# Kernel optimization log

Measured on AMD Instinct MI355X. Metric: run time of the kernel, lower is better.

## Reference

```python
import jax, jax.numpy as jnp
import numpy as np

N_POI = 100000   # number of POIs
N_EDGE = 50000   # directed hyperedges
N_USER = 50000   # user hyperedges (multi-view)
NNZ = 1_000_000  # nonzeros per incidence matrix
D = 128          # embedding dim
L = 3            # num_layers


def spmm(rows, cols, vals, x, num_rows):
    """COO sparse @ dense: y[r] += vals * x[c]."""
    return jax.ops.segment_sum(vals[:, None] * x[cols], rows, num_segments=num_rows)


def hyper_net(pois, rows1, cols1, vals1, n1, rows2, cols2, vals2, n2, attn):
    """Chained two-hop sparse propagation with relu + residual, layer-attention fusion.
    Dropout omitted (eval mode / deterministic reference)."""
    embs = [pois]
    x = pois
    for _ in range(L):
        m = spmm(rows1, cols1, vals1, x, n1)      # [n1, D] aggregate to hyperedges/users
        m = spmm(rows2, cols2, vals2, m, n2)      # [N_POI, D] propagate back to POIs
        x = jax.nn.relu(m) + embs[-1]             # relu + residual
        embs.append(x)
    w = jax.nn.softmax(attn)                      # [L+1]
    return jnp.einsum('l,lnd->nd', w, jnp.stack(embs))


def setup_inputs() -> dict:
    key = jax.random.key(0)
    ks = jax.random.split(key, 16)
    inp = {
        'pois_embs': jax.random.normal(ks[0], (N_POI, D), dtype=jnp.float32),
        'tar_rows': jax.random.randint(ks[1], (NNZ,), 0, N_EDGE, dtype=jnp.int32),
        'tar_cols': jax.random.randint(ks[2], (NNZ,), 0, N_POI, dtype=jnp.int32),
        'tar_vals': jax.random.uniform(ks[3], (NNZ,), dtype=jnp.float32),
        'src_rows': jax.random.randint(ks[4], (NNZ,), 0, N_POI, dtype=jnp.int32),
        'src_cols': jax.random.randint(ks[5], (NNZ,), 0, N_EDGE, dtype=jnp.int32),
        'src_vals': jax.random.uniform(ks[6], (NNZ,), dtype=jnp.float32),
        'up_rows': jax.random.randint(ks[7], (NNZ,), 0, N_USER, dtype=jnp.int32),
        'up_cols': jax.random.randint(ks[8], (NNZ,), 0, N_POI, dtype=jnp.int32),
        'up_vals': jax.random.uniform(ks[9], (NNZ,), dtype=jnp.float32),
        'pu_rows': jax.random.randint(ks[10], (NNZ,), 0, N_POI, dtype=jnp.int32),
        'pu_cols': jax.random.randint(ks[11], (NNZ,), 0, N_USER, dtype=jnp.int32),
        'pu_vals': jax.random.uniform(ks[12], (NNZ,), dtype=jnp.float32),
        'attn_di': jnp.ones((L + 1,), dtype=jnp.float32),
        'attn_mv': jnp.ones((L + 1,), dtype=jnp.float32),
    }
    return inp


def reference(pois_embs, tar_rows, tar_cols, tar_vals, src_rows, src_cols, src_vals,
              up_rows, up_cols, up_vals, pu_rows, pu_cols, pu_vals, attn_di, attn_mv):
    # Directed hypergraph branch: msg_tar = HG_poi_tar @ x ; msg_src = HG_poi_src @ msg_tar
    di = hyper_net(pois_embs, tar_rows, tar_cols, tar_vals, N_EDGE,
                   src_rows, src_cols, src_vals, N_POI, attn_di)
    # Multi-view (user) hypergraph branch: HG_up @ x ; HG_pu @ msg
    mv = hyper_net(pois_embs, up_rows, up_cols, up_vals, N_USER,
                   pu_rows, pu_cols, pu_vals, N_POI, attn_mv)
    return di + mv
```

## Files before the change

### kernel.cpp

```cpp
#include <hip/hip_runtime.h>

#define NNZC   1000000
#define NPOI   100000
#define NEDGE  50000
#define NUSER  50000
#define DIM    128
#define NL     3

#define PB     128
#define NBKT   196
#define SCANN  (4 * NBKT * PB)

static inline int ceil_div(int a, int b) { return (a + b - 1) / b; }

typedef unsigned int uint32;

__device__ __forceinline__ float bfLO(uint32 u) { return __uint_as_float(u << 16); }
__device__ __forceinline__ float bfHI(uint32 u) { return __uint_as_float(u & 0xffff0000u); }
__device__ __forceinline__ uint32 bf16_rne(float f) {
    uint32 u = __float_as_uint(f);
    return (u + 0x7fffu + ((u >> 16) & 1u)) >> 16;
}
__device__ __forceinline__ uint32 bfPACK(float a, float b) {
    return bf16_rne(a) | (bf16_rne(b) << 16);
}
__device__ __forceinline__ uint32 csrPACK(int col, float val) {
    return ((uint32)col) | (bf16_rne(val) << 17);
}
__device__ __forceinline__ int   csrCOL(uint32 e) { return (int)(e & 0x1FFFFu); }
__device__ __forceinline__ float csrVAL(uint32 e) { return __uint_as_float((e >> 17) << 16); }

__device__ __constant__ const int c_nrows[4]  = { NEDGE, NPOI, NUSER, NPOI };
__device__ __constant__ const int c_cntoff[4] = { 0, NEDGE, NEDGE + NPOI, NEDGE + NPOI + NUSER };
__device__ __constant__ const int c_cap[4]    = { 64, 48, 64, 48 };
__device__ __constant__ const int c_shift[4]  = { 8, 9, 8, 9 };
__device__ __constant__ const long long c_elloff[4] = { 0, 3200000, 8000000, 11200000 };


__global__ __launch_bounds__(1024) void histH_kernel(
    const int* __restrict__ r0, const int* __restrict__ r1,
    const int* __restrict__ r2, const int* __restrict__ r3,
    int* __restrict__ histG) {
    __shared__ int h[NBKT];
    int m = blockIdx.y, p = blockIdx.x;
    for (int i = threadIdx.x; i < NBKT; i += 1024) h[i] = 0;
    __syncthreads();
    const int* r = (m == 0) ? r0 : (m == 1) ? r1 : (m == 2) ? r2 : r3;
    int shift = c_shift[m];
    int lo = (int)(((long long)NNZC * p) >> 7);
    int hi = (int)(((long long)NNZC * (p + 1)) >> 7);
    for (int i = lo + (int)threadIdx.x; i < hi; i += 1024)
        atomicAdd(&h[r[i] >> shift], 1);
    __syncthreads();
    for (int b = threadIdx.x; b < NBKT; b += 1024)
        histG[(m * NBKT + b) * PB + p] = h[b];
}

__global__ __launch_bounds__(256) void scan_kernel(int* __restrict__ g) {
    __shared__ int base[257];
    int t = threadIdx.x;
    const int chunk = SCANN / 256;
    int lo = t * chunk;
    int s = 0;
    for (int i = 0; i < chunk; i++) s += g[lo + i];
    base[t + 1] = s;
    __syncthreads();
    if (t == 0) {
        base[0] = 0;
        for (int i = 1; i <= 256; i++) base[i] += base[i - 1];
    }
    __syncthreads();
    int off = base[t];
    for (int i = 0; i < chunk; i++) { int v = g[lo + i]; g[lo + i] = off; off += v; }
    if (t == 255) g[SCANN] = base[256];
}

__global__ __launch_bounds__(1024) void scatS_kernel(
    const int* __restrict__ r0, const int* __restrict__ r1,
    const int* __restrict__ r2, const int* __restrict__ r3,
    const int* __restrict__ c0, const int* __restrict__ c1,
    const int* __restrict__ c2, const int* __restrict__ c3,
    const float* __restrict__ v0, const float* __restrict__ v1,
    const float* __restrict__ v2, const float* __restrict__ v3,
    const int* __restrict__ scanG, uint2* __restrict__ rec) {
    __shared__ int cur[NBKT];
    int m = blockIdx.y, p = blockIdx.x;
    for (int b = threadIdx.x; b < NBKT; b += 1024)
        cur[b] = scanG[(m * NBKT + b) * PB + p];
    __syncthreads();
    const int*   r = (m == 0) ? r0 : (m == 1) ? r1 : (m == 2) ? r2 : r3;
    const int*   c = (m == 0) ? c0 : (m == 1) ? c1 : (m == 2) ? c2 : c3;
    const float* v = (m == 0) ? v0 : (m == 1) ? v1 : (m == 2) ? v2 : v3;
    int shift = c_shift[m];
    int lo = (int)(((long long)NNZC * p) >> 7);
    int hi = (int)(((long long)NNZC * (p + 1)) >> 7);
    for (int i = lo + (int)threadIdx.x; i < hi; i += 1024) {
        int row = r[i];
        int pos = atomicAdd(&cur[row >> shift], 1);
        rec[pos] = make_uint2((uint32)row, csrPACK(c[i], v[i]));
    }
}

__global__ __launch_bounds__(512) void fillB_kernel(
    const int* __restrict__ scanG, const uint2* __restrict__ rec,
    int* __restrict__ counts_all, uint32* __restrict__ ell) {
    __shared__ int cnt[512];
    int bx = (int)blockIdx.x;
    int m = bx / NBKT, b = bx - m * NBKT;
    int shift = c_shift[m];
    int rowlo = b << shift;
    int bklen = 1 << shift;
    for (int i = threadIdx.x; i < bklen; i += 512) cnt[i] = 0;
    __syncthreads();
    int lo = scanG[(m * NBKT + b) * PB];
    int hi = scanG[(m * NBKT + b + 1) * PB];
    int cap = c_cap[m];
    uint32* ebase = ell + c_elloff[m];
    for (int i = lo + (int)threadIdx.x; i < hi; i += 512) {
        uint2 e = rec[i];
        int row = (int)e.x;
        int pos = atomicAdd(&cnt[row - rowlo], 1);
        ebase[(size_t)row * cap + pos] = e.y;
    }
    __syncthreads();
    int nrows_b = c_nrows[m] - rowlo;
    if (nrows_b > bklen) nrows_b = bklen;
    int* counts = counts_all + c_cntoff[m];
    for (int i = threadIdx.x; i < nrows_b; i += 512)
        counts[rowlo + i] = cnt[i];
}

__global__ void softmax4_kernel(const float* __restrict__ adi,
                                const float* __restrict__ amv,
                                float* __restrict__ w) {
    if (blockIdx.x == 0 && threadIdx.x == 0) {
        for (int b = 0; b < 2; b++) {
            const float* a = b ? amv : adi;
            float m = a[0];
            for (int l = 1; l < 4; l++) m = fmaxf(m, a[l]);
            float e[4]; float s = 0.f;
            for (int l = 0; l < 4; l++) { e[l] = __expf(a[l] - m); s += e[l]; }
            for (int l = 0; l < 4; l++) w[b * 4 + l] = e[l] / s;
        }
    }
}

__global__ void cast_bf16_kernel(const float* __restrict__ src, uint32* __restrict__ dst, int npairs) {
    int i = blockIdx.x * blockDim.x + threadIdx.x;
    if (i < npairs) {
        float2 f = *(const float2*)(src + (size_t)i * 2);
        dst[i] = bfPACK(f.x, f.y);
    }
}

#define GPROC(E, U) do { float _v = csrVAL(E); \
    acc.x = fmaf(_v, bfLO(U), acc.x); acc.y = fmaf(_v, bfHI(U), acc.y); } while (0)

template<int CAP>
__global__ __launch_bounds__(256) void spmm1_kernel(
    const int* __restrict__ counts, const uint32* __restrict__ ell,
    const uint32* __restrict__ xbf, uint32* __restrict__ ybf, int n_rows) {
    int row = (int)((blockIdx.x * blockDim.x + threadIdx.x) >> 6);
    int lane = (int)(threadIdx.x & 63);
    if (row >= n_rows) return;
    row = __builtin_amdgcn_readfirstlane(row);
    int cnt = __builtin_amdgcn_readfirstlane(counts[row]);
    const uint32* erow = ell + row * CAP;
    const uint4*  erow4 = (const uint4*)erow;
    float2 acc = make_float2(0.f, 0.f);
    int j = 0;
    for (; j + 8 <= cnt; j += 8) {
        uint4 qa = erow4[j >> 2], qb = erow4[(j >> 2) + 1];
        uint32 u0 = xbf[csrCOL(qa.x) * 64 + lane];
        uint32 u1 = xbf[csrCOL(qa.y) * 64 + lane];
        uint32 u2 = xbf[csrCOL(qa.z) * 64 + lane];
        uint32 u3 = xbf[csrCOL(qa.w) * 64 + lane];
        uint32 u4 = xbf[csrCOL(qb.x) * 64 + lane];
        uint32 u5 = xbf[csrCOL(qb.y) * 64 + lane];
        uint32 u6 = xbf[csrCOL(qb.z) * 64 + lane];
        uint32 u7 = xbf[csrCOL(qb.w) * 64 + lane];
        GPROC(qa.x, u0); GPROC(qa.y, u1); GPROC(qa.z, u2); GPROC(qa.w, u3);
        GPROC(qb.x, u4); GPROC(qb.y, u5); GPROC(qb.z, u6); GPROC(qb.w, u7);
    }
    for (; j + 4 <= cnt; j += 4) {
        uint4 q = erow4[j >> 2];
        uint32 u0 = xbf[csrCOL(q.x) * 64 + lane];
        uint32 u1 = xbf[csrCOL(q.y) * 64 + lane];
        uint32 u2 = xbf[csrCOL(q.z) * 64 + lane];
        uint32 u3 = xbf[csrCOL(q.w) * 64 + lane];
        GPROC(q.x, u0); GPROC(q.y, u1); GPROC(q.z, u2); GPROC(q.w, u3);
    }
    for (; j < cnt; j++) {
        uint32 e = erow[j];
        uint32 u = xbf[csrCOL(e) * 64 + lane];
        GPROC(e, u);
    }
    ybf[row * 64 + lane] = bfPACK(acc.x, acc.y);
}

template<int CAP>
__global__ __launch_bounds__(256) void spmm2_kernel(
    const int* __restrict__ counts, const uint32* __restrict__ ell,
    const uint32* __restrict__ mbf, const uint32* __restrict__ xinbf,
    uint32* __restrict__ xoutbf, int n_rows) {
    int row = (int)((blockIdx.x * blockDim.x + threadIdx.x) >> 6);
    int lane = (int)(threadIdx.x & 63);
    if (row >= n_rows) return;
    row = __builtin_amdgcn_readfirstlane(row);
    int cnt = __builtin_amdgcn_readfirstlane(counts[row]);
    const uint32* erow = ell + row * CAP;
    const uint4*  erow4 = (const uint4*)erow;
    float2 acc = make_float2(0.f, 0.f);
    int j = 0;
    for (; j + 8 <= cnt; j += 8) {
        uint4 qa = erow4[j >> 2], qb = erow4[(j >> 2) + 1];
        uint32 u0 = mbf[csrCOL(qa.x) * 64 + lane];
        uint32 u1 = mbf[csrCOL(qa.y) * 64 + lane];
        uint32 u2 = mbf[csrCOL(qa.z) * 64 + lane];
        uint32 u3 = mbf[csrCOL(qa.w) * 64 + lane];
        uint32 u4 = mbf[csrCOL(qb.x) * 64 + lane];
        uint32 u5 = mbf[csrCOL(qb.y) * 64 + lane];
        uint32 u6 = mbf[csrCOL(qb.z) * 64 + lane];
        uint32 u7 = mbf[csrCOL(qb.w) * 64 + lane];
        GPROC(qa.x, u0); GPROC(qa.y, u1); GPROC(qa.z, u2); GPROC(qa.w, u3);
        GPROC(qb.x, u4); GPROC(qb.y, u5); GPROC(qb.z, u6); GPROC(qb.w, u7);
    }
    for (; j + 4 <= cnt; j += 4) {
        uint4 q = erow4[j >> 2];
        uint32 u0 = mbf[csrCOL(q.x) * 64 + lane];
        uint32 u1 = mbf[csrCOL(q.y) * 64 + lane];
        uint32 u2 = mbf[csrCOL(q.z) * 64 + lane];
        uint32 u3 = mbf[csrCOL(q.w) * 64 + lane];
        GPROC(q.x, u0); GPROC(q.y, u1); GPROC(q.z, u2); GPROC(q.w, u3);
    }
    for (; j < cnt; j++) {
        uint32 e = erow[j];
        uint32 u = mbf[csrCOL(e) * 64 + lane];
        GPROC(e, u);
    }
    int o32 = row * 64 + lane;
    uint32 ui = xinbf[o32];
    float xn0 = fmaxf(acc.x, 0.f) + bfLO(ui);
    float xn1 = fmaxf(acc.y, 0.f) + bfHI(ui);
    xoutbf[o32] = bfPACK(xn0, xn1);
}

__global__ void epi1_kernel(const float* __restrict__ pois,
                            const uint32* __restrict__ x1, const uint32* __restrict__ x2,
                            const uint32* __restrict__ x3, const float* __restrict__ w,
                            float* __restrict__ out) {
    int i = blockIdx.x * blockDim.x + threadIdx.x;
    if (i < NPOI * 64) {
        float w0 = w[0] + w[4];
        float2 pf = ((const float2*)pois)[i];
        uint32 u1 = x1[i], u2 = x2[i], u3 = x3[i];
        float o0 = w0 * pf.x + w[1] * bfLO(u1) + w[2] * bfLO(u2) + w[3] * bfLO(u3);
        float o1 = w0 * pf.y + w[1] * bfHI(u1) + w[2] * bfHI(u2) + w[3] * bfHI(u3);
        ((float2*)out)[i] = make_float2(o0, o1);
    }
}

__global__ void epi2_kernel(const uint32* __restrict__ x1, const uint32* __restrict__ x2,
                            const uint32* __restrict__ x3, const float* __restrict__ w,
                            float* __restrict__ out) {
    int i = blockIdx.x * blockDim.x + threadIdx.x;
    if (i < NPOI * 64) {
        uint32 u1 = x1[i], u2 = x2[i], u3 = x3[i];
        float2 ov = ((float2*)out)[i];
        ov.x += w[5] * bfLO(u1) + w[6] * bfLO(u2) + w[7] * bfLO(u3);
        ov.y += w[5] * bfHI(u1) + w[6] * bfHI(u2) + w[7] * bfHI(u3);
        ((float2*)out)[i] = ov;
    }
}

extern "C" void kernel_launch(void* const* d_in, const int* in_sizes, int n_in,
                              void* d_out, int out_size, void* d_ws, size_t ws_size,
                              hipStream_t stream) {
    const float* pois = (const float*)d_in[0];
    const int*   rows_in[4] = { (const int*)d_in[1], (const int*)d_in[4],
                                (const int*)d_in[7], (const int*)d_in[10] };
    const int*   cols_in[4] = { (const int*)d_in[2], (const int*)d_in[5],
                                (const int*)d_in[8], (const int*)d_in[11] };
    const float* vals_in[4] = { (const float*)d_in[3], (const float*)d_in[6],
                                (const float*)d_in[9], (const float*)d_in[12] };
    const float* attn_di = (const float*)d_in[13];
    const float* attn_mv = (const float*)d_in[14];
    float* out = (float*)d_out;

    const int NTOT = NEDGE + NPOI + NUSER + NPOI;
    const int cnt_off[4] = { 0, NEDGE, NEDGE + NPOI, NEDGE + NPOI + NUSER };
    const long long ell_off[4] = { 0, 3200000, 8000000, 11200000 };

    char* p = (char*)d_ws;
    float*  wsoft      = (float*)p;  p += 256;
    int*    counts_all = (int*)p;    p += (size_t)NTOT * 4;
    p = (char*)(((size_t)p + 255) & ~255ull);
    int*    scanG      = (int*)p;    p += (size_t)(SCANN + 64) * 4;
    p = (char*)(((size_t)p + 255) & ~255ull);
    uint32* ell        = (uint32*)p; p += (size_t)16000000 * 4;
    uint32* mbf        = (uint32*)p; p += (size_t)NEDGE * 64 * 4;
    uint32* poisbf     = (uint32*)p; p += (size_t)NPOI * 64 * 4;
    uint32* xl[3];
    for (int l = 0; l < 3; l++) { xl[l] = (uint32*)p; p += (size_t)NPOI * 64 * 4; }
    uint2* rec = (uint2*)xl[0];
    (void)ws_size; (void)out_size; (void)n_in; (void)in_sizes;

    histH_kernel<<<dim3(PB, 4), 1024, 0, stream>>>(
        rows_in[0], rows_in[1], rows_in[2], rows_in[3], scanG);
    scan_kernel<<<1, 256, 0, stream>>>(scanG);
    scatS_kernel<<<dim3(PB, 4), 1024, 0, stream>>>(
        rows_in[0], rows_in[1], rows_in[2], rows_in[3],
        cols_in[0], cols_in[1], cols_in[2], cols_in[3],
        vals_in[0], vals_in[1], vals_in[2], vals_in[3],
        scanG, rec);
    fillB_kernel<<<4 * NBKT, 512, 0, stream>>>(scanG, rec, counts_all, ell);

    softmax4_kernel<<<1, 64, 0, stream>>>(attn_di, attn_mv, wsoft);
    cast_bf16_kernel<<<ceil_div(NPOI * 64, 256), 256, 0, stream>>>(pois, poisbf, NPOI * 64);

    for (int br = 0; br < 2; br++) {
        int m1i = br ? 2 : 0;
        int m2i = br ? 3 : 1;
        const int* cn1 = counts_all + cnt_off[m1i];
        const int* cn2 = counts_all + cnt_off[m2i];
        const uint32* el1 = ell + ell_off[m1i];
        const uint32* el2 = ell + ell_off[m2i];
        const int n1 = 50000;
        const uint32* xcur = poisbf;
        for (int l = 1; l <= NL; l++) {
            spmm1_kernel<64><<<ceil_div(n1, 4), 256, 0, stream>>>(cn1, el1, xcur, mbf, n1);
            spmm2_kernel<48><<<ceil_div(NPOI, 4), 256, 0, stream>>>(
                cn2, el2, mbf, xcur, xl[l - 1], NPOI);
            xcur = xl[l - 1];
        }
        if (br == 0)
            epi1_kernel<<<ceil_div(NPOI * 64, 256), 256, 0, stream>>>(
                pois, xl[0], xl[1], xl[2], wsoft, out);
        else
            epi2_kernel<<<ceil_div(NPOI * 64, 256), 256, 0, stream>>>(
                xl[0], xl[1], xl[2], wsoft, out);
    }
}
```

Measured before the change: 790.9 us.

## Map 16 threads per row with 128-bit gathers in SpMM kernels; halve preprocessing partitions

The SpMM kernels now assign 16 lanes per sparse row instead of a full 64-lane wavefront, and each lane loads a uint4 (8 bf16 values) per gathered neighbor row, giving four rows per wavefront. This cuts the number of load instructions per nonzero and raises how many rows are in flight at once, aiming to hide gather latency better. Rows with different nonzero counts now share a wavefront, so divergence can rise, and the scalar readfirstlane handling of row and count is lost. Separately, the histogram and scatter preprocessing uses 64 partitions per matrix instead of 128.

```diff
diff --git a/kernel.cpp b/kernel.cpp
--- a/kernel.cpp
+++ b/kernel.cpp
@@ -7,7 +7,7 @@
 #define DIM    128
 #define NL     3
 
-#define PB     128
+#define PB     64
 #define NBKT   196
 #define SCANN  (4 * NBKT * PB)
 
@@ -47,8 +47,8 @@
     __syncthreads();
     const int* r = (m == 0) ? r0 : (m == 1) ? r1 : (m == 2) ? r2 : r3;
     int shift = c_shift[m];
-    int lo = (int)(((long long)NNZC * p) >> 7);
-    int hi = (int)(((long long)NNZC * (p + 1)) >> 7);
+    int lo = (int)(((long long)NNZC * p) >> 6);
+    int hi = (int)(((long long)NNZC * (p + 1)) >> 6);
     for (int i = lo + (int)threadIdx.x; i < hi; i += 1024)
         atomicAdd(&h[r[i] >> shift], 1);
     __syncthreads();
@@ -92,8 +92,8 @@
     const int*   c = (m == 0) ? c0 : (m == 1) ? c1 : (m == 2) ? c2 : c3;
     const float* v = (m == 0) ? v0 : (m == 1) ? v1 : (m == 2) ? v2 : v3;
     int shift = c_shift[m];
-    int lo = (int)(((long long)NNZC * p) >> 7);
-    int hi = (int)(((long long)NNZC * (p + 1)) >> 7);
+    int lo = (int)(((long long)NNZC * p) >> 6);
+    int hi = (int)(((long long)NNZC * (p + 1)) >> 6);
     for (int i = lo + (int)threadIdx.x; i < hi; i += 1024) {
         int row = r[i];
         int pos = atomicAdd(&cur[row >> shift], 1);
@@ -153,49 +153,59 @@
     }
 }
 
-#define GPROC(E, U) do { float _v = csrVAL(E); \
-    acc.x = fmaf(_v, bfLO(U), acc.x); acc.y = fmaf(_v, bfHI(U), acc.y); } while (0)
+__device__ __forceinline__ void fma8(float2& a0, float2& a1, float2& a2, float2& a3,
+                                     float v, uint4 u) {
+    a0.x = fmaf(v, bfLO(u.x), a0.x); a0.y = fmaf(v, bfHI(u.x), a0.y);
+    a1.x = fmaf(v, bfLO(u.y), a1.x); a1.y = fmaf(v, bfHI(u.y), a1.y);
+    a2.x = fmaf(v, bfLO(u.z), a2.x); a2.y = fmaf(v, bfHI(u.z), a2.y);
+    a3.x = fmaf(v, bfLO(u.w), a3.x); a3.y = fmaf(v, bfHI(u.w), a3.y);
+}
 
 template<int CAP>
 __global__ __launch_bounds__(256) void spmm1_kernel(
     const int* __restrict__ counts, const uint32* __restrict__ ell,
     const uint32* __restrict__ xbf, uint32* __restrict__ ybf, int n_rows) {
-    int row = (int)((blockIdx.x * blockDim.x + threadIdx.x) >> 6);
-    int lane = (int)(threadIdx.x & 63);
+    int row = (int)((blockIdx.x * blockDim.x + threadIdx.x) >> 4);
+    int t   = (int)(threadIdx.x & 15);
     if (row >= n_rows) return;
-    row = __builtin_amdgcn_readfirstlane(row);
-    int cnt = __builtin_amdgcn_readfirstlane(counts[row]);
-    const uint32* erow = ell + row * CAP;
-    const uint4*  erow4 = (const uint4*)erow;
-    float2 acc = make_float2(0.f, 0.f);
+    int cnt = counts[row];
+    const uint32* erow = ell + (size_t)row * CAP;
+    float2 a0 = {0.f,0.f}, a1 = {0.f,0.f}, a2 = {0.f,0.f}, a3 = {0.f,0.f};
     int j = 0;
     for (; j + 8 <= cnt; j += 8) {
-        uint4 qa = erow4[j >> 2], qb = erow4[(j >> 2) + 1];
-        uint32 u0 = xbf[csrCOL(qa.x) * 64 + lane];
-        uint32 u1 = xbf[csrCOL(qa.y) * 64 + lane];
-        uint32 u2 = xbf[csrCOL(qa.z) * 64 + lane];
-        uint32 u3 = xbf[csrCOL(qa.w) * 64 + lane];
-        uint32 u4 = xbf[csrCOL(qb.x) * 64 + lane];
-        uint32 u5 = xbf[csrCOL(qb.y) * 64 + lane];
-        uint32 u6 = xbf[csrCOL(qb.z) * 64 + lane];
-        uint32 u7 = xbf[csrCOL(qb.w) * 64 + lane];
-        GPROC(qa.x, u0); GPROC(qa.y, u1); GPROC(qa.z, u2); GPROC(qa.w, u3);
-        GPROC(qb.x, u4); GPROC(qb.y, u5); GPROC(qb.z, u6); GPROC(qb.w, u7);
+        uint4 qa = *(const uint4*)(erow + j);
+        uint4 qb = *(const uint4*)(erow + j + 4);
+        uint4 u0 = *((const uint4*)(xbf + (size_t)csrCOL(qa.x) * 64) + t);
+        uint4 u1 = *((const uint4*)(xbf + (size_t)csrCOL(qa.y) * 64) + t);
+        uint4 u2 = *((const uint4*)(xbf + (size_t)csrCOL(qa.z) * 64) + t);
+        uint4 u3 = *((const uint4*)(xbf + (size_t)csrCOL(qa.w) * 64) + t);
+        uint4 u4 = *((const uint4*)(xbf + (size_t)csrCOL(qb.x) * 64) + t);
+        uint4 u5 = *((const uint4*)(xbf + (size_t)csrCOL(qb.y) * 64) + t);
+        uint4 u6 = *((const uint4*)(xbf + (size_t)csrCOL(qb.z) * 64) + t);
+        uint4 u7 = *((const uint4*)(xbf + (size_t)csrCOL(qb.w) * 64) + t);
+        fma8(a0,a1,a2,a3, csrVAL(qa.x), u0); fma8(a0,a1,a2,a3, csrVAL(qa.y), u1);
+        fma8(a0,a1,a2,a3, csrVAL(qa.z), u2); fma8(a0,a1,a2,a3, csrVAL(qa.w), u3);
+        fma8(a0,a1,a2,a3, csrVAL(qb.x), u4); fma8(a0,a1,a2,a3, csrVAL(qb.y), u5);
+        fma8(a0,a1,a2,a3, csrVAL(qb.z), u6); fma8(a0,a1,a2,a3, csrVAL(qb.w), u7);
     }
     for (; j + 4 <= cnt; j += 4) {
-        uint4 q = erow4[j >> 2];
-        uint32 u0 = xbf[csrCOL(q.x) * 64 + lane];
-        uint32 u1 = xbf[csrCOL(q.y) * 64 + lane];
-        uint32 u2 = xbf[csrCOL(q.z) * 64 + lane];
-        uint32 u3 = xbf[csrCOL(q.w) * 64 + lane];
-        GPROC(q.x, u0); GPROC(q.y, u1); GPROC(q.z, u2); GPROC(q.w, u3);
+        uint4 q = *(const uint4*)(erow + j);
+        uint4 u0 = *((const uint4*)(xbf + (size_t)csrCOL(q.x) * 64) + t);
+        uint4 u1 = *((const uint4*)(xbf + (size_t)csrCOL(q.y) * 64) + t);
+        uint4 u2 = *((const uint4*)(xbf + (size_t)csrCOL(q.z) * 64) + t);
+        uint4 u3 = *((const uint4*)(xbf + (size_t)csrCOL(q.w) * 64) + t);
+        fma8(a0,a1,a2,a3, csrVAL(q.x), u0); fma8(a0,a1,a2,a3, csrVAL(q.y), u1);
+        fma8(a0,a1,a2,a3, csrVAL(q.z), u2); fma8(a0,a1,a2,a3, csrVAL(q.w), u3);
     }
     for (; j < cnt; j++) {
         uint32 e = erow[j];
-        uint32 u = xbf[csrCOL(e) * 64 + lane];
-        GPROC(e, u);
-    }
-    ybf[row * 64 + lane] = bfPACK(acc.x, acc.y);
+        uint4 u = *((const uint4*)(xbf + (size_t)csrCOL(e) * 64) + t);
+        fma8(a0,a1,a2,a3, csrVAL(e), u);
+    }
+    uint4 o;
+    o.x = bfPACK(a0.x, a0.y); o.y = bfPACK(a1.x, a1.y);
+    o.z = bfPACK(a2.x, a2.y); o.w = bfPACK(a3.x, a3.y);
+    *((uint4*)(ybf + (size_t)row * 64) + t) = o;
 }
 
 template<int CAP>
@@ -203,46 +213,50 @@
     const int* __restrict__ counts, const uint32* __restrict__ ell,
     const uint32* __restrict__ mbf, const uint32* __restrict__ xinbf,
     uint32* __restrict__ xoutbf, int n_rows) {
-    int row = (int)((blockIdx.x * blockDim.x + threadIdx.x) >> 6);
-    int lane = (int)(threadIdx.x & 63);
+    int row = (int)((blockIdx.x * blockDim.x + threadIdx.x) >> 4);
+    int t   = (int)(threadIdx.x & 15);
     if (row >= n_rows) return;
-    row = __builtin_amdgcn_readfirstlane(row);
-    int cnt = __builtin_amdgcn_readfirstlane(counts[row]);
-    const uint32* erow = ell + row * CAP;
-    const uint4*  erow4 = (const uint4*)erow;
-    float2 acc = make_float2(0.f, 0.f);
+    int cnt = counts[row];
+    const uint32* erow = ell + (size_t)row * CAP;
+    float2 a0 = {0.f,0.f}, a1 = {0.f,0.f}, a2 = {0.f,0.f}, a3 = {0.f,0.f};
     int j = 0;
     for (; j + 8 <= cnt; j += 8) {
-        uint4 qa = erow4[j >> 2], qb = erow4[(j >> 2) + 1];
-        uint32 u0 = mbf[csrCOL(qa.x) * 64 + lane];
-        uint32 u1 = mbf[csrCOL(qa.y) * 64 + lane];
-        uint32 u2 = mbf[csrCOL(qa.z) * 64 + lane];
-        uint32 u3 = mbf[csrCOL(qa.w) * 64 + lane];
-        uint32 u4 = mbf[csrCOL(qb.x) * 64 + lane];
-        uint32 u5 = mbf[csrCOL(qb.y) * 64 + lane];
-        uint32 u6 = mbf[csrCOL(qb.z) * 64 + lane];
-        uint32 u7 = mbf[csrCOL(qb.w) * 64 + lane];
-        GPROC(qa.x, u0); GPROC(qa.y, u1); GPROC(qa.z, u2); GPROC(qa.w, u3);
-        GPROC(qb.x, u4); GPROC(qb.y, u5); GPROC(qb.z, u6); GPROC(qb.w, u7);
+        uint4 qa = *(const uint4*)(erow + j);
+        uint4 qb = *(const uint4*)(erow + j + 4);
+        uint4 u0 = *((const uint4*)(mbf + (size_t)csrCOL(qa.x) * 64) + t);
+        uint4 u1 = *((const uint4*)(mbf + (size_t)csrCOL(qa.y) * 64) + t);
+        uint4 u2 = *((const uint4*)(mbf + (size_t)csrCOL(qa.z) * 64) + t);
+        uint4 u3 = *((const uint4*)(mbf + (size_t)csrCOL(qa.w) * 64) + t);
+        uint4 u4 = *((const uint4*)(mbf + (size_t)csrCOL(qb.x) * 64) + t);
+        uint4 u5 = *((const uint4*)(mbf + (size_t)csrCOL(qb.y) * 64) + t);
+        uint4 u6 = *((const uint4*)(mbf + (size_t)csrCOL(qb.z) * 64) + t);
+        uint4 u7 = *((const uint4*)(mbf + (size_t)csrCOL(qb.w) * 64) + t);
+        fma8(a0,a1,a2,a3, csrVAL(qa.x), u0); fma8(a0,a1,a2,a3, csrVAL(qa.y), u1);
+        fma8(a0,a1,a2,a3, csrVAL(qa.z), u2); fma8(a0,a1,a2,a3, csrVAL(qa.w), u3);
+        fma8(a0,a1,a2,a3, csrVAL(qb.x), u4); fma8(a0,a1,a2,a3, csrVAL(qb.y), u5);
+        fma8(a0,a1,a2,a3, csrVAL(qb.z), u6); fma8(a0,a1,a2,a3, csrVAL(qb.w), u7);
     }
     for (; j + 4 <= cnt; j += 4) {
-        uint4 q = erow4[j >> 2];
-        uint32 u0 = mbf[csrCOL(q.x) * 64 + lane];
-        uint32 u1 = mbf[csrCOL(q.y) * 64 + lane];
-        uint32 u2 = mbf[csrCOL(q.z) * 64 + lane];
-        uint32 u3 = mbf[csrCOL(q.w) * 64 + lane];
-        GPROC(q.x, u0); GPROC(q.y, u1); GPROC(q.z, u2); GPROC(q.w, u3);
+        uint4 q = *(const uint4*)(erow + j);
+        uint4 u0 = *((const uint4*)(mbf + (size_t)csrCOL(q.x) * 64) + t);
+        uint4 u1 = *((const uint4*)(mbf + (size_t)csrCOL(q.y) * 64) + t);
+        uint4 u2 = *((const uint4*)(mbf + (size_t)csrCOL(q.z) * 64) + t);
+        uint4 u3 = *((const uint4*)(mbf + (size_t)csrCOL(q.w) * 64) + t);
+        fma8(a0,a1,a2,a3, csrVAL(q.x), u0); fma8(a0,a1,a2,a3, csrVAL(q.y), u1);
+        fma8(a0,a1,a2,a3, csrVAL(q.z), u2); fma8(a0,a1,a2,a3, csrVAL(q.w), u3);
     }
     for (; j < cnt; j++) {
         uint32 e = erow[j];
-        uint32 u = mbf[csrCOL(e) * 64 + lane];
-        GPROC(e, u);
-    }
-    int o32 = row * 64 + lane;
-    uint32 ui = xinbf[o32];
-    float xn0 = fmaxf(acc.x, 0.f) + bfLO(ui);
-    float xn1 = fmaxf(acc.y, 0.f) + bfHI(ui);
-    xoutbf[o32] = bfPACK(xn0, xn1);
+        uint4 u = *((const uint4*)(mbf + (size_t)csrCOL(e) * 64) + t);
+        fma8(a0,a1,a2,a3, csrVAL(e), u);
+    }
+    uint4 ui = *((const uint4*)(xinbf + (size_t)row * 64) + t);
+    uint4 o;
+    o.x = bfPACK(fmaxf(a0.x, 0.f) + bfLO(ui.x), fmaxf(a0.y, 0.f) + bfHI(ui.x));
+    o.y = bfPACK(fmaxf(a1.x, 0.f) + bfLO(ui.y), fmaxf(a1.y, 0.f) + bfHI(ui.y));
+    o.z = bfPACK(fmaxf(a2.x, 0.f) + bfLO(ui.z), fmaxf(a2.y, 0.f) + bfHI(ui.z));
+    o.w = bfPACK(fmaxf(a3.x, 0.f) + bfLO(ui.w), fmaxf(a3.y, 0.f) + bfHI(ui.w));
+    *((uint4*)(xoutbf + (size_t)row * 64) + t) = o;
 }
 
 __global__ void epi1_kernel(const float* __restrict__ pois,
@@ -328,8 +342,8 @@
         const int n1 = 50000;
         const uint32* xcur = poisbf;
         for (int l = 1; l <= NL; l++) {
-            spmm1_kernel<64><<<ceil_div(n1, 4), 256, 0, stream>>>(cn1, el1, xcur, mbf, n1);
-            spmm2_kernel<48><<<ceil_div(NPOI, 4), 256, 0, stream>>>(
+            spmm1_kernel<64><<<ceil_div(n1, 16), 256, 0, stream>>>(cn1, el1, xcur, mbf, n1);
+            spmm2_kernel<48><<<ceil_div(NPOI, 16), 256, 0, stream>>>(
                 cn2, el2, mbf, xcur, xl[l - 1], NPOI);
             xcur = xl[l - 1];
         }
```

Result: no change. 778.0 us (-1.6%).
